# Kernel optimization log

Measured on AMD Instinct MI355X. Metric: run time of the kernel, lower is better.

The kernel has to match this reference:

```python
import jax, jax.numpy as jnp
import numpy as np
from jax import lax

N_CLASSES = 10
N_EXPERTS = 45  # 10 choose 2
EPS = 1e-5

# lookup table: (i1, i2) with i1 < i2 -> flat expert id (matches nested loop order)
_tbl = np.zeros((N_CLASSES, N_CLASSES), dtype=np.int32)
_k = 0
for _i1 in range(N_CLASSES):
    for _i2 in range(_i1 + 1, N_CLASSES):
        _tbl[_i1, _i2] = _k
        _k += 1
PAIR_TABLE = jnp.asarray(_tbl)


def _downscale(x):
    # AvgPool2d(3, stride=3) on 28x28 -> 9x9 (floor: uses top-left 27x27)
    B = x.shape[0]
    return x[:, :, :27, :27].reshape(B, 1, 9, 3, 9, 3).mean(axis=(3, 5))


def _bn_eval(h, gamma, beta, mean, var):
    scale = gamma * lax.rsqrt(var + EPS)
    return h * scale[None, :, None, None] + (beta - mean * scale)[None, :, None, None]


def _stage1(x, w1, b1, g1, be1, m1, v1, fcw1, fcb1):
    xd = _downscale(x)                                         # [B,1,9,9]
    h = lax.conv_general_dilated(xd, w1, (1, 1), 'VALID',
                                 dimension_numbers=('NCHW', 'OIHW', 'NCHW'))
    h = h + b1[None, :, None, None]                            # [B,20,7,7]
    h = _bn_eval(h, g1, be1, m1, v1)
    h = jax.nn.relu(h)
    B = h.shape[0]
    h = h[:, :, :6, :6].reshape(B, 20, 3, 2, 3, 2).max(axis=(3, 5))  # maxpool2 -> [B,20,3,3]
    h = h.reshape(B, 180)
    return h @ fcw1.T + fcb1                                   # [B,10] raw logits


def reference(x, w1, b1, g1, be1, m1, v1, fcw1, fcb1,
              w2, b2, g2, be2, m2, v2, fcw2, fcb2):
    B = x.shape[0]
    logits1 = _stage1(x, w1, b1, g1, be1, m1, v1, fcw1, fcb1)  # [B,10]
    ls1 = jax.nn.log_softmax(logits1, axis=1)

    # routing: top-2 class indices, sorted ascending, -> pairwise expert id
    top2 = jnp.sort(jnp.argsort(ls1, axis=1)[:, -2:], axis=1)  # [B,2]
    idx0, idx1 = top2[:, 0], top2[:, 1]
    eid = PAIR_TABLE[idx0, idx1]                               # [B]

    # stage 2 (TinyNet2) with per-example gathered expert params
    xd = _downscale(x)                                         # [B,1,9,9]
    # extract 5x5 conv patches (valid, stride 1): output spatial 5x5
    patches = jnp.stack([xd[:, 0, i:i + 5, j:j + 5]
                         for i in range(5) for j in range(5)], axis=1)  # [B,25,5,5]
    Wsel = w2.reshape(N_EXPERTS, 15, 25)[eid]                  # [B,15,25]
    h = jnp.einsum('bkhw,bok->bohw', patches, Wsel) + b2[eid][:, :, None, None]  # [B,15,5,5]
    scale = (g2 * lax.rsqrt(v2 + EPS))[eid]                    # [B,15]
    shift = (be2 - m2 * g2 * lax.rsqrt(v2 + EPS))[eid]
    h = h * scale[:, :, None, None] + shift[:, :, None, None]
    h = jax.nn.relu(h)
    h = h[:, :, :4, :4].reshape(B, 15, 2, 2, 2, 2).max(axis=(3, 5))  # [B,15,2,2]
    feat = h.reshape(B, 60)
    s2 = jnp.einsum('bf,bof->bo', feat, fcw2[eid]) + fcb2[eid]  # [B,2]

    # combine: scatter the two expert logits into the routed columns
    rows = jnp.arange(B)
    out = jnp.full((B, N_CLASSES), -100.0, dtype=logits1.dtype)
    out = out.at[rows, idx0].set(s2[:, 0]).at[rows, idx1].set(s2[:, 1])
    # eval-mode bypass: use stage1 raw logits if max log-prob > 0.3
    use1 = jnp.max(ls1, axis=1) > 0.3
    out = jnp.where(use1[:, None], logits1, out)
    out = jax.nn.log_softmax(out, axis=1)
    return (logits1, out)


def setup_inputs() -> dict:
    key = jax.random.key(0)
    ks = jax.random.split(key, 18)
    B = 65536
    s = 0.1
    return {
        'x': jax.random.normal(ks[0], (B, 1, 28, 28), dtype=jnp.float32),
        # stage1 (TinyNet, 20 kernels, k=3)
        'w1': jax.random.normal(ks[1], (20, 1, 3, 3), dtype=jnp.float32) * s,
        'b1': jax.random.normal(ks[2], (20,), dtype=jnp.float32) * s,
        'g1': jax.random.normal(ks[3], (20,), dtype=jnp.float32) * s + 1.0,
        'be1': jax.random.normal(ks[4], (20,), dtype=jnp.float32) * s,
        'm1': jax.random.normal(ks[5], (20,), dtype=jnp.float32) * s,
        'v1': jax.random.uniform(ks[6], (20,), dtype=jnp.float32) + 0.5,
        'fcw1': jax.random.normal(ks[7], (10, 180), dtype=jnp.float32) * s,
        'fcb1': jax.random.normal(ks[8], (10,), dtype=jnp.float32) * s,
        # 45 stacked stage2 experts (TinyNet2, 15 kernels, k=5)
        'w2': jax.random.normal(ks[9], (45, 15, 1, 5, 5), dtype=jnp.float32) * s,
        'b2': jax.random.normal(ks[10], (45, 15), dtype=jnp.float32) * s,
        'g2': jax.random.normal(ks[11], (45, 15), dtype=jnp.float32) * s + 1.0,
        'be2': jax.random.normal(ks[12], (45, 15), dtype=jnp.float32) * s,
        'm2': jax.random.normal(ks[13], (45, 15), dtype=jnp.float32) * s,
        'v2': jax.random.uniform(ks[14], (45, 15), dtype=jnp.float32) + 0.5,
        'fcw2': jax.random.normal(ks[15], (45, 2, 60), dtype=jnp.float32) * s,
        'fcb2': jax.random.normal(ks[16], (45, 2), dtype=jnp.float32) * s,
    }
```

## Files before the change

### kernel.cpp

```cpp
#include <hip/hip_runtime.h>
#include <cmath>

#define EPSF 1e-5f

#define OFF_FC2   19576
#define OFF_IMG   25088

#define I_W1P    0
#define I_FCW1R  240
#define I_B1F    2400
#define I_FCB1   2420
#define I_B2F    2432
#define I_FCB2   3108

__global__ __launch_bounds__(256) void setup_tables(
    const float* __restrict__ w1, const float* __restrict__ b1,
    const float* __restrict__ g1, const float* __restrict__ be1,
    const float* __restrict__ m1, const float* __restrict__ v1,
    const float* __restrict__ w2, const float* __restrict__ b2,
    const float* __restrict__ g2, const float* __restrict__ be2,
    const float* __restrict__ m2, const float* __restrict__ v2,
    const float* __restrict__ fcw2, const float* __restrict__ fcb2,
    const float* __restrict__ fcw1, const float* __restrict__ fcb1,
    float* __restrict__ ws)
{
  const int t  = blockIdx.x * blockDim.x + threadIdx.x;
  const int nt = gridDim.x * blockDim.x;
  float* W2F = ws;
  float* FC2 = ws + OFF_FC2;
  float* IMG = ws + OFF_IMG;

  for (int idx = t; idx < 18900; idx += nt) {
    int kk = idx & 3, rest = idx >> 2;
    int e = rest % 45, ok4 = rest / 45;
    int k4 = ok4 % 7, o = ok4 / 7;
    int k = k4 * 4 + kk;
    float s = g2[e*15+o] / sqrtf(v2[e*15+o] + EPSF);
    W2F[idx] = (k < 25) ? w2[(e*15+o)*25 + k] * s : 0.0f;
  }
  for (int idx = t; idx < 5400; idx += nt) {
    int kk = idx & 3, rest = idx >> 2;
    int e = rest % 45, t2 = rest / 45;
    int f4 = t2 % 15, oo = t2 / 15;
    FC2[idx] = fcw2[(e*2+oo)*60 + f4*4 + kk];
  }
  for (int i = t; i < 4096; i += nt) {
    float v = 0.0f;
    if (i < I_FCW1R) {
      int ch = i / 12, j = i % 12;
      if (j < 9) {
        float s = g1[ch] / sqrtf(v1[ch] + EPSF);
        v = w1[ch*9 + j] * s;
      }
    } else if (i < I_B1F) {
      int k = i - I_FCW1R;
      int c = k % 12, r2 = k / 12, pp = r2 % 9, ch = r2 / 9;
      if (c < 10) v = fcw1[c*180 + ch*9 + pp];
    } else if (i < I_FCB1) {
      int ch = i - I_B1F;
      float s = g1[ch] / sqrtf(v1[ch] + EPSF);
      v = b1[ch]*s + be1[ch] - m1[ch]*s;
    } else if (i < I_B2F) {
      int k = i - I_FCB1;
      if (k < 10) v = fcb1[k];
    } else if (i < I_FCB2) {
      int k = i - I_B2F;
      if (k < 675) {
        int e = k % 45, o = k / 45;
        float s = g2[e*15+o] / sqrtf(v2[e*15+o] + EPSF);
        v = b2[e*15+o]*s + be2[e*15+o] - m2[e*15+o]*s;
      }
    } else {
      int k = i - I_FCB2;
      if (k < 90) {
        int e = k % 45, oo = k / 45;
        v = fcb2[e*2+oo];
      }
    }
    IMG[i] = v;
  }
}

#define GETC(arr, k) ((k)%4==0 ? arr[(k)/4].x : (k)%4==1 ? arr[(k)/4].y : \
                      (k)%4==2 ? arr[(k)/4].z : arr[(k)/4].w)

#define T_TAB 4352

__global__ __attribute__((amdgpu_waves_per_eu(2, 4))) __launch_bounds__(256)
void fused_k(
    const float* __restrict__ x,
    const float* __restrict__ ws,
    float* __restrict__ out, int B)
{
  __shared__ float lds[8448];

  const int t  = threadIdx.x;
  const int p  = t & 3;
  const int sl = t >> 2;
  const int b  = blockIdx.x * 64 + sl;
  const bool valid = (b < B);

  const float4* img4 = reinterpret_cast<const float4*>(ws + OFF_IMG);
  float4 tv0 = img4[t], tv1 = img4[t + 256], tv2 = img4[t + 512], tv3 = img4[t + 768];

  if (valid) {
    const float* xb = x + (size_t)b * 784;
    #pragma unroll
    for (int ri = 0; ri < 2; ri++) {
      const int r = 2*p + ri;
      float4 rowv[3][6];
      #pragma unroll
      for (int dr = 0; dr < 3; dr++) {
        const float4* rv = reinterpret_cast<const float4*>(xb + (3*r + dr) * 28);
        #pragma unroll
        for (int q = 0; q < 6; q++) rowv[dr][q] = rv[q];
      }
      float d[8];
      #pragma unroll
      for (int c = 0; c < 8; c++) {
        float s = 0.0f;
        #pragma unroll
        for (int dr = 0; dr < 3; dr++)
          s += GETC(rowv[dr], 3*c) + GETC(rowv[dr], 3*c+1) + GETC(rowv[dr], 3*c+2);
        d[c] = s * (1.0f / 9.0f);
      }
      float4* dst = reinterpret_cast<float4*>(&lds[sl*68 + r*8]);
      dst[0] = make_float4(d[0], d[1], d[2], d[3]);
      dst[1] = make_float4(d[4], d[5], d[6], d[7]);
    }
  }
  {
    float4* tab4 = reinterpret_cast<float4*>(&lds[T_TAB]);
    tab4[t] = tv0; tab4[t + 256] = tv1; tab4[t + 512] = tv2; tab4[t + 768] = tv3;
  }
  __syncthreads();

  float xd[64];
  #pragma unroll
  for (int r = 0; r < 8; r++) {
    const float4* src = reinterpret_cast<const float4*>(&lds[sl*68 + r*8]);
    float4 a = src[0], bq = src[1];
    xd[r*8+0]=a.x;  xd[r*8+1]=a.y;  xd[r*8+2]=a.z;  xd[r*8+3]=a.w;
    xd[r*8+4]=bq.x; xd[r*8+5]=bq.y; xd[r*8+6]=bq.z; xd[r*8+7]=bq.w;
  }

  float logits[10];
  #pragma unroll
  for (int c = 0; c < 10; c++) logits[c] = 0.0f;

  #pragma unroll 1
  for (int ci = 0; ci < 5; ci++) {
    const int ch = p*5 + ci;
    const float4* wp = reinterpret_cast<const float4*>(&lds[T_TAB + I_W1P + ch*12]);
    float4 w0 = wp[0], w1v = wp[1], w2v = wp[2];
    const float w_[9] = {w0.x,w0.y,w0.z,w0.w,w1v.x,w1v.y,w1v.z,w1v.w,w2v.x};
    const float bb = lds[T_TAB + I_B1F + ch];
    float feat[9];
    #pragma unroll
    for (int pr = 0; pr < 3; pr++) {
      #pragma unroll
      for (int pc = 0; pc < 3; pc++) {
        float c00 = bb, c01 = bb, c10 = bb, c11 = bb;
        #pragma unroll
        for (int dr = 0; dr < 3; dr++) {
          #pragma unroll
          for (int dc = 0; dc < 3; dc++) {
            float wk = w_[dr*3 + dc];
            c00 = fmaf(xd[(2*pr+0+dr)*8 + 2*pc+0+dc], wk, c00);
            c01 = fmaf(xd[(2*pr+0+dr)*8 + 2*pc+1+dc], wk, c01);
            c10 = fmaf(xd[(2*pr+1+dr)*8 + 2*pc+0+dc], wk, c10);
            c11 = fmaf(xd[(2*pr+1+dr)*8 + 2*pc+1+dc], wk, c11);
          }
        }
        feat[pr*3+pc] = fmaxf(fmaxf(fmaxf(c00, c01), fmaxf(c10, c11)), 0.0f);
      }
    }
    #pragma unroll
    for (int pp = 0; pp < 9; pp++) {
      const float4* f4 = reinterpret_cast<const float4*>(&lds[T_TAB + I_FCW1R + (ch*9 + pp)*12]);
      float4 f0 = f4[0], f1 = f4[1], f2 = f4[2];
      const float fv = feat[pp];
      logits[0] = fmaf(fv, f0.x, logits[0]);
      logits[1] = fmaf(fv, f0.y, logits[1]);
      logits[2] = fmaf(fv, f0.z, logits[2]);
      logits[3] = fmaf(fv, f0.w, logits[3]);
      logits[4] = fmaf(fv, f1.x, logits[4]);
      logits[5] = fmaf(fv, f1.y, logits[5]);
      logits[6] = fmaf(fv, f1.z, logits[6]);
      logits[7] = fmaf(fv, f1.w, logits[7]);
      logits[8] = fmaf(fv, f2.x, logits[8]);
      logits[9] = fmaf(fv, f2.y, logits[9]);
    }
  }

  #pragma unroll
  for (int c = 0; c < 10; c++) {
    float v = logits[c];
    v += __shfl_xor(v, 1);
    v += __shfl_xor(v, 2);
    logits[c] = v + lds[T_TAB + I_FCB1 + c];
  }

  int i1 = 0; float v1m = logits[0];
  #pragma unroll
  for (int c = 1; c < 10; c++) { if (logits[c] >= v1m) { v1m = logits[c]; i1 = c; } }
  int i2 = 0; float v2m = -3.0e38f;
  #pragma unroll
  for (int c = 0; c < 10; c++) { if (c != i1 && logits[c] >= v2m) { v2m = logits[c]; i2 = c; } }
  const int idx0 = i1 < i2 ? i1 : i2;
  const int idx1 = i1 < i2 ? i2 : i1;
  int eid = 8*idx0 - (idx0*(idx0-1))/2 + idx1 - 1;
  eid = eid < 0 ? 0 : (eid > 44 ? 44 : eid);

  float sume = 0.0f;
  #pragma unroll
  for (int c = 0; c < 10; c++) sume += __expf(logits[c] - v1m);
  const bool use1 = (-__logf(sume)) > 0.3f;

  __syncthreads();
  if (p == 0) {
    #pragma unroll
    for (int c = 0; c < 5; c++) lds[sl*10 + c] = logits[c];
  } else if (p == 1) {
    #pragma unroll
    for (int c = 5; c < 10; c++) lds[sl*10 + c] = logits[c];
  }

  const float4* W2F4 = reinterpret_cast<const float4*>(ws);
  const float4* FC24 = reinterpret_cast<const float4*>(ws + OFF_FC2);
  float s2a = 0.0f, s2b = 0.0f;

  #pragma unroll 1
  for (int oi = 0; oi < 4; oi++) {
    const int o = p + 4*oi;
    if (o < 15) {
      float4 wv[7];
      #pragma unroll
      for (int k4 = 0; k4 < 7; k4++) wv[k4] = W2F4[(o*7 + k4)*45 + eid];
      const float bias = lds[T_TAB + I_B2F + o*45 + eid];
      const float4 fa = FC24[o*45 + eid];
      const float4 fb = FC24[(15 + o)*45 + eid];
      float feat0 = 0.f, feat1 = 0.f, feat2 = 0.f, feat3 = 0.f;
      #pragma unroll
      for (int ph = 0; ph < 2; ph++) {
        #pragma unroll
        for (int pw = 0; pw < 2; pw++) {
          float c00 = bias, c01 = bias, c10 = bias, c11 = bias;
          #pragma unroll
          for (int i = 0; i < 5; i++) {
            #pragma unroll
            for (int j = 0; j < 5; j++) {
              float wk = GETC(wv, i*5 + j);
              c00 = fmaf(xd[(2*ph+0+i)*8 + 2*pw+0+j], wk, c00);
              c01 = fmaf(xd[(2*ph+0+i)*8 + 2*pw+1+j], wk, c01);
              c10 = fmaf(xd[(2*ph+1+i)*8 + 2*pw+0+j], wk, c10);
              c11 = fmaf(xd[(2*ph+1+i)*8 + 2*pw+1+j], wk, c11);
            }
          }
          float f = fmaxf(fmaxf(fmaxf(c00, c01), fmaxf(c10, c11)), 0.0f);
          if (ph == 0 && pw == 0) feat0 = f;
          else if (ph == 0)       feat1 = f;
          else if (pw == 0)       feat2 = f;
          else                    feat3 = f;
        }
      }
      s2a = fmaf(feat0, fa.x, fmaf(feat1, fa.y, fmaf(feat2, fa.z, fmaf(feat3, fa.w, s2a))));
      s2b = fmaf(feat0, fb.x, fmaf(feat1, fb.y, fmaf(feat2, fb.z, fmaf(feat3, fb.w, s2b))));
    }
  }
  s2a += __shfl_xor(s2a, 1); s2a += __shfl_xor(s2a, 2);
  s2b += __shfl_xor(s2b, 1); s2b += __shfl_xor(s2b, 2);
  s2a += lds[T_TAB + I_FCB2 + eid];
  s2b += lds[T_TAB + I_FCB2 + 45 + eid];

  __syncthreads();
  float o10[10];
  #pragma unroll
  for (int c = 0; c < 10; c++) {
    float v = -100.0f;
    v = (c == idx0) ? s2a : v;
    v = (c == idx1) ? s2b : v;
    o10[c] = use1 ? lds[sl*10 + c] : v;
  }
  float m2x = o10[0];
  #pragma unroll
  for (int c = 1; c < 10; c++) m2x = fmaxf(m2x, o10[c]);
  float se2 = 0.0f;
  #pragma unroll
  for (int c = 0; c < 10; c++) se2 += __expf(o10[c] - m2x);
  const float lse2 = m2x + __logf(se2);

  if (p == 2) {
    #pragma unroll
    for (int c = 0; c < 5; c++) lds[640 + sl*10 + c] = o10[c] - lse2;
  } else if (p == 3) {
    #pragma unroll
    for (int c = 5; c < 10; c++) lds[640 + sl*10 + c] = o10[c] - lse2;
  }
  __syncthreads();

  if (blockIdx.x * 64 + 64 <= B) {
    const float4* l4 = reinterpret_cast<const float4*>(lds);
    const size_t o1 = (size_t)blockIdx.x * 640;
    if (t < 160)
      *reinterpret_cast<float4*>(out + o1 + (size_t)t*4) = l4[t];
    if (t >= 96)
      *reinterpret_cast<float4*>(out + (size_t)B*10 + o1 + (size_t)(t-96)*4) = l4[160 + (t-96)];
  } else if (valid) {
    const size_t base = (size_t)b * 10;
    if (p == 0) {
      #pragma unroll
      for (int c = 0; c < 5; c++) out[base + c] = lds[sl*10 + c];
    } else if (p == 1) {
      #pragma unroll
      for (int c = 5; c < 10; c++) out[base + c] = lds[sl*10 + c];
    } else if (p == 2) {
      #pragma unroll
      for (int c = 0; c < 5; c++) out[(size_t)B*10 + base + c] = lds[640 + sl*10 + c];
    } else {
      #pragma unroll
      for (int c = 5; c < 10; c++) out[(size_t)B*10 + base + c] = lds[640 + sl*10 + c];
    }
  }
}

extern "C" void kernel_launch(void* const* d_in, const int* in_sizes, int n_in,
                              void* d_out, int out_size, void* d_ws, size_t ws_size,
                              hipStream_t stream) {
  const float* x    = (const float*)d_in[0];
  const float* w1   = (const float*)d_in[1];
  const float* b1   = (const float*)d_in[2];
  const float* g1   = (const float*)d_in[3];
  const float* be1  = (const float*)d_in[4];
  const float* m1   = (const float*)d_in[5];
  const float* v1   = (const float*)d_in[6];
  const float* fcw1 = (const float*)d_in[7];
  const float* fcb1 = (const float*)d_in[8];
  const float* w2   = (const float*)d_in[9];
  const float* b2   = (const float*)d_in[10];
  const float* g2   = (const float*)d_in[11];
  const float* be2  = (const float*)d_in[12];
  const float* m2   = (const float*)d_in[13];
  const float* v2   = (const float*)d_in[14];
  const float* fcw2 = (const float*)d_in[15];
  const float* fcb2 = (const float*)d_in[16];
  float* out = (float*)d_out;
  float* ws  = (float*)d_ws;
  const int B = in_sizes[0] / 784;

  setup_tables<<<80, 256, 0, stream>>>(w1, b1, g1, be1, m1, v1,
                                       w2, b2, g2, be2, m2, v2,
                                       fcw2, fcb2, fcw1, fcb1, ws);
  fused_k<<<(B + 63)/64, 256, 0, stream>>>(x, ws, out, B);
}
```

Baseline: 334.4 us.

## Stage input images through LDS with coalesced double-buffered loads, read tables from global

The per-sample strided row loads are replaced with coalesced float4 loads of 8 whole images at a time into an LDS staging area. The 3x3 average pooling is then computed from LDS, and the next chunk's global loads are prefetched in registers while the current chunk is pooled. The constant tables are no longer copied into LDS and are read directly from global or cache. This trades many block-wide barriers and larger LDS use, which may lower occupancy, for better global coalescing, and it makes the table reads hit global memory instead of LDS.

```diff
diff --git a/kernel.cpp b/kernel.cpp
--- a/kernel.cpp
+++ b/kernel.cpp
@@ -84,7 +84,8 @@
 #define GETC(arr, k) ((k)%4==0 ? arr[(k)/4].x : (k)%4==1 ? arr[(k)/4].y : \
                       (k)%4==2 ? arr[(k)/4].z : arr[(k)/4].w)
 
-#define T_TAB 4352
+#define T_RAW   4352
+#define SSTR    676
 
 __global__ __attribute__((amdgpu_waves_per_eu(2, 4))) __launch_bounds__(256)
 void fused_k(
@@ -92,7 +93,7 @@
     const float* __restrict__ ws,
     float* __restrict__ out, int B)
 {
-  __shared__ float lds[8448];
+  __shared__ float lds[9760];
 
   const int t  = threadIdx.x;
   const int p  = t & 3;
@@ -100,40 +101,68 @@
   const int b  = blockIdx.x * 64 + sl;
   const bool valid = (b < B);
 
-  const float4* img4 = reinterpret_cast<const float4*>(ws + OFF_IMG);
-  float4 tv0 = img4[t], tv1 = img4[t + 256], tv2 = img4[t + 512], tv3 = img4[t + 768];
-
-  if (valid) {
-    const float* xb = x + (size_t)b * 784;
-    #pragma unroll
-    for (int ri = 0; ri < 2; ri++) {
-      const int r = 2*p + ri;
-      float4 rowv[3][6];
+  const float* IMG = ws + OFF_IMG;
+
+  const int s8  = t >> 5;
+  const int tin = t & 31;
+
+  float4 pre[6];
+  {
+    const int bs = blockIdx.x * 64 + s8;
+    if (bs < B) {
+      const float4* xp = reinterpret_cast<const float4*>(x + (size_t)bs * 784);
+      #pragma unroll
+      for (int j = 0; j < 5; j++) pre[j] = xp[tin + 32*j];
+      pre[5] = (tin < 8) ? xp[tin + 160] : make_float4(0.f,0.f,0.f,0.f);
+    } else {
+      #pragma unroll
+      for (int j = 0; j < 6; j++) pre[j] = make_float4(0.f,0.f,0.f,0.f);
+    }
+    float4* rw = reinterpret_cast<float4*>(&lds[T_RAW + s8*SSTR]);
+    #pragma unroll
+    for (int j = 0; j < 5; j++) rw[tin + 32*j] = pre[j];
+    if (tin < 8) rw[tin + 160] = pre[5];
+  }
+  __syncthreads();
+
+  #pragma unroll 1
+  for (int c = 0; c < 8; c++) {
+    if (c < 7) {
+      const int bs = blockIdx.x * 64 + (c+1)*8 + s8;
+      if (bs < B) {
+        const float4* xp = reinterpret_cast<const float4*>(x + (size_t)bs * 784);
+        #pragma unroll
+        for (int j = 0; j < 5; j++) pre[j] = xp[tin + 32*j];
+        pre[5] = (tin < 8) ? xp[tin + 160] : make_float4(0.f,0.f,0.f,0.f);
+      }
+    }
+    if (t < 128) {
+      const int ds8  = t >> 4;
+      const int orow = (t >> 1) & 7;
+      const int h    = t & 1;
+      float a0 = 0.f, a1 = 0.f, a2 = 0.f, a3 = 0.f;
       #pragma unroll
       for (int dr = 0; dr < 3; dr++) {
-        const float4* rv = reinterpret_cast<const float4*>(xb + (3*r + dr) * 28);
-        #pragma unroll
-        for (int q = 0; q < 6; q++) rowv[dr][q] = rv[q];
-      }
-      float d[8];
-      #pragma unroll
-      for (int c = 0; c < 8; c++) {
-        float s = 0.0f;
-        #pragma unroll
-        for (int dr = 0; dr < 3; dr++)
-          s += GETC(rowv[dr], 3*c) + GETC(rowv[dr], 3*c+1) + GETC(rowv[dr], 3*c+2);
-        d[c] = s * (1.0f / 9.0f);
-      }
-      float4* dst = reinterpret_cast<float4*>(&lds[sl*68 + r*8]);
-      dst[0] = make_float4(d[0], d[1], d[2], d[3]);
-      dst[1] = make_float4(d[4], d[5], d[6], d[7]);
-    }
-  }
-  {
-    float4* tab4 = reinterpret_cast<float4*>(&lds[T_TAB]);
-    tab4[t] = tv0; tab4[t + 256] = tv1; tab4[t + 512] = tv2; tab4[t + 768] = tv3;
-  }
-  __syncthreads();
+        const float4* rp = reinterpret_cast<const float4*>(
+            &lds[T_RAW + ds8*SSTR + (3*orow + dr)*28 + 12*h]);
+        float4 q0 = rp[0], q1 = rp[1], q2 = rp[2];
+        a0 += q0.x + q0.y + q0.z;
+        a1 += q0.w + q1.x + q1.y;
+        a2 += q1.z + q1.w + q2.x;
+        a3 += q2.y + q2.z + q2.w;
+      }
+      float4* dst = reinterpret_cast<float4*>(&lds[(c*8 + ds8)*68 + orow*8 + 4*h]);
+      *dst = make_float4(a0*(1.f/9.f), a1*(1.f/9.f), a2*(1.f/9.f), a3*(1.f/9.f));
+    }
+    __syncthreads();
+    if (c < 7) {
+      float4* rw = reinterpret_cast<float4*>(&lds[T_RAW + s8*SSTR]);
+      #pragma unroll
+      for (int j = 0; j < 5; j++) rw[tin + 32*j] = pre[j];
+      if (tin < 8) rw[tin + 160] = pre[5];
+      __syncthreads();
+    }
+  }
 
   float xd[64];
   #pragma unroll
@@ -151,10 +180,10 @@
   #pragma unroll 1
   for (int ci = 0; ci < 5; ci++) {
     const int ch = p*5 + ci;
-    const float4* wp = reinterpret_cast<const float4*>(&lds[T_TAB + I_W1P + ch*12]);
+    const float4* wp = reinterpret_cast<const float4*>(IMG + I_W1P + ch*12);
     float4 w0 = wp[0], w1v = wp[1], w2v = wp[2];
     const float w_[9] = {w0.x,w0.y,w0.z,w0.w,w1v.x,w1v.y,w1v.z,w1v.w,w2v.x};
-    const float bb = lds[T_TAB + I_B1F + ch];
+    const float bb = IMG[I_B1F + ch];
     float feat[9];
     #pragma unroll
     for (int pr = 0; pr < 3; pr++) {
@@ -177,7 +206,7 @@
     }
     #pragma unroll
     for (int pp = 0; pp < 9; pp++) {
-      const float4* f4 = reinterpret_cast<const float4*>(&lds[T_TAB + I_FCW1R + (ch*9 + pp)*12]);
+      const float4* f4 = reinterpret_cast<const float4*>(IMG + I_FCW1R + (ch*9 + pp)*12);
       float4 f0 = f4[0], f1 = f4[1], f2 = f4[2];
       const float fv = feat[pp];
       logits[0] = fmaf(fv, f0.x, logits[0]);
@@ -198,7 +227,7 @@
     float v = logits[c];
     v += __shfl_xor(v, 1);
     v += __shfl_xor(v, 2);
-    logits[c] = v + lds[T_TAB + I_FCB1 + c];
+    logits[c] = v + IMG[I_FCB1 + c];
   }
 
   int i1 = 0; float v1m = logits[0];
@@ -237,7 +266,7 @@
       float4 wv[7];
       #pragma unroll
       for (int k4 = 0; k4 < 7; k4++) wv[k4] = W2F4[(o*7 + k4)*45 + eid];
-      const float bias = lds[T_TAB + I_B2F + o*45 + eid];
+      const float bias = IMG[I_B2F + o*45 + eid];
       const float4 fa = FC24[o*45 + eid];
       const float4 fb = FC24[(15 + o)*45 + eid];
       float feat0 = 0.f, feat1 = 0.f, feat2 = 0.f, feat3 = 0.f;
@@ -270,8 +299,8 @@
   }
   s2a += __shfl_xor(s2a, 1); s2a += __shfl_xor(s2a, 2);
   s2b += __shfl_xor(s2b, 1); s2b += __shfl_xor(s2b, 2);
-  s2a += lds[T_TAB + I_FCB2 + eid];
-  s2b += lds[T_TAB + I_FCB2 + 45 + eid];
+  s2a += IMG[I_FCB2 + eid];
+  s2b += IMG[I_FCB2 + 45 + eid];
 
   __syncthreads();
   float o10[10];
```

Measured after the change: 369.2 us. 10.4% more time.
